# Kernel optimization log

Measured on AMD Instinct MI355X. Metric: run time of the kernel, lower is better.

## Reference

```python
import jax, jax.numpy as jnp
import numpy as np

E = 16          # ensemble_size
S = 64          # state_size
A = 32          # action_size
R = 1           # reward_size
I = S + A       # combined input size
HS = 64         # SubModel_state hidden
HR = 32         # SubModel_reward hidden
B = 16384       # batch


def setup_inputs() -> dict:
    key = jax.random.key(0)
    ks = jax.random.split(key, 10)

    def init_lin(k, fan_in, shape):
        bound = 1.0 / np.sqrt(fan_in)
        return jax.random.uniform(k, shape, jnp.float32, -bound, bound)

    return {
        "state": jax.random.normal(ks[0], (B, S), jnp.float32),
        "action": jax.random.normal(ks[1], (B, A), jnp.float32),
        # stacked ensemble state-model weights (torch Linear stores [out,in]; we use [in,out])
        "W1": init_lin(ks[2], I, (E, I, HS)),
        "b1": init_lin(ks[3], I, (E, HS)),
        "W2": init_lin(ks[4], HS, (E, HS, S)),
        "b2": init_lin(ks[5], HS, (E, S)),
        # stacked ensemble reward-model weights
        "rW1": init_lin(ks[6], I, (E, I, HR)),
        "rb1": init_lin(ks[7], I, (E, HR)),
        "rW2": init_lin(ks[8], HR, (E, HR, R)),
        "rb2": init_lin(ks[9], HR, (E, R)),
    }


def reference(state, action, W1, b1, W2, b2, rW1, rb1, rW2, rb2):
    x = jnp.concatenate([state, action], axis=1)  # [B, I]
    # state models: Linear -> ReLU -> Linear, all ensemble members in one batched GEMM
    h = jax.nn.relu(jnp.einsum("bi,eih->ebh", x, W1) + b1[:, None, :])  # [E, B, HS]
    pred_states = jnp.einsum("ebh,ehs->ebs", h, W2) + b2[:, None, :]    # [E, B, S]
    # reward models: Linear -> ReLU -> Linear -> clamp(-100, 200)
    hr = jax.nn.relu(jnp.einsum("bi,eih->ebh", x, rW1) + rb1[:, None, :])  # [E, B, HR]
    pred_rewards = jnp.einsum("ebh,ehr->ebr", hr, rW2) + rb2[:, None, :]   # [E, B, R]
    pred_rewards = jnp.clip(pred_rewards, -100.0, 200.0)
    return (pred_states, pred_rewards)
```

## Files before the change

### kernel.cpp

```cpp
#include <hip/hip_runtime.h>
#include <hip/hip_bf16.h>
#include <cstdint>
#include <cstddef>

#define Bsz 16384
#define Esz 16
#define Ssz 64
#define Asz 32
#define Isz 96
#define HSz 64
#define HRz 32

#define NTM 256
#define CHUNK 512
#define NTILE 8

typedef __attribute__((ext_vector_type(8))) short bf16x8;
typedef __attribute__((ext_vector_type(4))) short short4v;
typedef __attribute__((ext_vector_type(4))) float f32x4;

static __device__ __forceinline__ short f2bf(float f) {
    __hip_bfloat16 b = __float2bfloat16(f);
    return *reinterpret_cast<short*>(&b);
}
static __device__ __forceinline__ float bf2f(short s) {
    union { uint32_t u; float f; } v; v.u = ((uint32_t)(uint16_t)s) << 16; return v.f;
}
static __device__ __forceinline__ bf16x8 pack8(float4 lo, float4 hi) {
    bf16x8 r;
    r[0] = f2bf(lo.x); r[1] = f2bf(lo.y); r[2] = f2bf(lo.z); r[3] = f2bf(lo.w);
    r[4] = f2bf(hi.x); r[5] = f2bf(hi.y); r[6] = f2bf(hi.z); r[7] = f2bf(hi.w);
    return r;
}

__global__ __launch_bounds__(NTM, 2)
void fused_all(const float* __restrict__ state, const float* __restrict__ action,
               const float* __restrict__ W1, const float* __restrict__ b1,
               const float* __restrict__ W2, const float* __restrict__ b2,
               const float* __restrict__ rW1, const float* __restrict__ rb1,
               const float* __restrict__ rW2, const float* __restrict__ rb2,
               float* __restrict__ outS, float* __restrict__ outR)
{
    __shared__ __align__(16) short HT[4][16][68];

    const int bid = blockIdx.x;
    const int xcd = bid & 7;
    const int rem = bid >> 3;
    const int e   = rem & (Esz - 1);
    const int c0  = (xcd + 8 * (rem >> 4)) * CHUNK;

    const int w = threadIdx.x >> 6, lane = threadIdx.x & 63;
    const int lr = lane & 15, lg = lane >> 4;

    bf16x8 w1r[4][3], rw1r[2][3], w2r[4][2];
    {
        const float* base = W1 + (size_t)e * Isz * HSz;
        #pragma unroll
        for (int nt = 0; nt < 4; ++nt)
            #pragma unroll
            for (int kk = 0; kk < 3; ++kk) {
                const float* p = base + (kk * 32 + lg * 8) * HSz + nt * 16 + lr;
                bf16x8 r;
                #pragma unroll
                for (int t = 0; t < 8; ++t) r[t] = f2bf(p[t * HSz]);
                w1r[nt][kk] = r;
            }
    }
    {
        const float* base = rW1 + (size_t)e * Isz * HRz;
        #pragma unroll
        for (int nt = 0; nt < 2; ++nt)
            #pragma unroll
            for (int kk = 0; kk < 3; ++kk) {
                const float* p = base + (kk * 32 + lg * 8) * HRz + nt * 16 + lr;
                bf16x8 r;
                #pragma unroll
                for (int t = 0; t < 8; ++t) r[t] = f2bf(p[t * HRz]);
                rw1r[nt][kk] = r;
            }
    }
    {
        const float* base = W2 + (size_t)e * HSz * Ssz;
        #pragma unroll
        for (int nt = 0; nt < 4; ++nt)
            #pragma unroll
            for (int kk = 0; kk < 2; ++kk) {
                const float* p = base + (kk * 32 + lg * 8) * Ssz + nt * 16 + lr;
                bf16x8 r;
                #pragma unroll
                for (int t = 0; t < 8; ++t) r[t] = f2bf(p[t * Ssz]);
                w2r[nt][kk] = r;
            }
    }

    short4v b1p[4], b2p[4], rb1p[2], rw2p[2];
    #pragma unroll
    for (int nt = 0; nt < 4; ++nt) {
        float4 v1 = *(const float4*)&b1[e * HSz + nt * 16 + lg * 4];
        float4 v2 = *(const float4*)&b2[e * Ssz + nt * 16 + lg * 4];
        b1p[nt] = (short4v){ f2bf(v1.x), f2bf(v1.y), f2bf(v1.z), f2bf(v1.w) };
        b2p[nt] = (short4v){ f2bf(v2.x), f2bf(v2.y), f2bf(v2.z), f2bf(v2.w) };
    }
    #pragma unroll
    for (int nt = 0; nt < 2; ++nt) {
        float4 v1 = *(const float4*)&rb1[e * HRz + nt * 16 + lg * 4];
        float4 v2 = *(const float4*)&rW2[e * HRz + nt * 16 + lg * 4];
        rb1p[nt] = (short4v){ f2bf(v1.x), f2bf(v1.y), f2bf(v1.z), f2bf(v1.w) };
        rw2p[nt] = (short4v){ f2bf(v2.x), f2bf(v2.y), f2bf(v2.z), f2bf(v2.w) };
    }
    const float rb2s = rb2[e];

    const int row0 = c0 + w * 16 + lr;
    const float* sbase = state  + (size_t)row0 * Ssz + lg * 8;
    const float* abase = action + (size_t)row0 * Asz + lg * 8;

    float4 xs0 = *(const float4*)(sbase);
    float4 xs1 = *(const float4*)(sbase + 4);
    float4 xs2 = *(const float4*)(sbase + 32);
    float4 xs3 = *(const float4*)(sbase + 36);
    float4 xa0 = *(const float4*)(abase);
    float4 xa1 = *(const float4*)(abase + 4);
    bf16x8 a0 = pack8(xs0, xs1);
    bf16x8 a1 = pack8(xs2, xs3);
    bf16x8 a2 = pack8(xa0, xa1);

    #pragma unroll 1
    for (int t = 0; t < NTILE; ++t) {
        const int tn = (t + 1) & (NTILE - 1);
        const float* sp = sbase + (size_t)tn * 64 * Ssz;
        const float* ap = abase + (size_t)tn * 64 * Asz;
        float4 ns0 = *(const float4*)(sp);
        float4 ns1 = *(const float4*)(sp + 4);
        float4 ns2 = *(const float4*)(sp + 32);
        float4 ns3 = *(const float4*)(sp + 36);
        float4 na0 = *(const float4*)(ap);
        float4 na1 = *(const float4*)(ap + 4);

        f32x4 accS[4];
        #pragma unroll
        for (int nt = 0; nt < 4; ++nt) {
            f32x4 acc = (f32x4){ bf2f(b1p[nt][0]), bf2f(b1p[nt][1]),
                                 bf2f(b1p[nt][2]), bf2f(b1p[nt][3]) };
            acc = __builtin_amdgcn_mfma_f32_16x16x32_bf16(w1r[nt][0], a0, acc, 0, 0, 0);
            acc = __builtin_amdgcn_mfma_f32_16x16x32_bf16(w1r[nt][1], a1, acc, 0, 0, 0);
            acc = __builtin_amdgcn_mfma_f32_16x16x32_bf16(w1r[nt][2], a2, acc, 0, 0, 0);
            accS[nt] = acc;
        }
        f32x4 accR[2];
        #pragma unroll
        for (int nt = 0; nt < 2; ++nt) {
            f32x4 acc = (f32x4){ bf2f(rb1p[nt][0]), bf2f(rb1p[nt][1]),
                                 bf2f(rb1p[nt][2]), bf2f(rb1p[nt][3]) };
            acc = __builtin_amdgcn_mfma_f32_16x16x32_bf16(rw1r[nt][0], a0, acc, 0, 0, 0);
            acc = __builtin_amdgcn_mfma_f32_16x16x32_bf16(rw1r[nt][1], a1, acc, 0, 0, 0);
            acc = __builtin_amdgcn_mfma_f32_16x16x32_bf16(rw1r[nt][2], a2, acc, 0, 0, 0);
            accR[nt] = acc;
        }

        #pragma unroll
        for (int nt = 0; nt < 4; ++nt) {
            short4v p = { f2bf(fmaxf(accS[nt][0], 0.f)),
                          f2bf(fmaxf(accS[nt][1], 0.f)),
                          f2bf(fmaxf(accS[nt][2], 0.f)),
                          f2bf(fmaxf(accS[nt][3], 0.f)) };
            *(short4v*)&HT[w][lr][nt * 16 + lg * 4] = p;
        }

        float rp = 0.f;
        #pragma unroll
        for (int nt = 0; nt < 2; ++nt) {
            rp += fmaxf(accR[nt][0], 0.f) * bf2f(rw2p[nt][0]);
            rp += fmaxf(accR[nt][1], 0.f) * bf2f(rw2p[nt][1]);
            rp += fmaxf(accR[nt][2], 0.f) * bf2f(rw2p[nt][2]);
            rp += fmaxf(accR[nt][3], 0.f) * bf2f(rw2p[nt][3]);
        }
        rp += __shfl_xor(rp, 16);
        rp += __shfl_xor(rp, 32);
        if (lane < 16)
            __builtin_nontemporal_store(fminf(fmaxf(rp + rb2s, -100.f), 200.f),
                                        &outR[(size_t)e * Bsz + row0 + t * 64]);

        bf16x8 h0 = *(const bf16x8*)&HT[w][lr][lg * 8];
        bf16x8 h1 = *(const bf16x8*)&HT[w][lr][32 + lg * 8];
        #pragma unroll
        for (int nt = 0; nt < 4; ++nt) {
            f32x4 acc = (f32x4){ bf2f(b2p[nt][0]), bf2f(b2p[nt][1]),
                                 bf2f(b2p[nt][2]), bf2f(b2p[nt][3]) };
            acc = __builtin_amdgcn_mfma_f32_16x16x32_bf16(w2r[nt][0], h0, acc, 0, 0, 0);
            acc = __builtin_amdgcn_mfma_f32_16x16x32_bf16(w2r[nt][1], h1, acc, 0, 0, 0);
            __builtin_nontemporal_store(acc,
                (f32x4*)&outS[((size_t)e * Bsz + row0 + t * 64) * Ssz + nt * 16 + lg * 4]);
        }

        a0 = pack8(ns0, ns1);
        a1 = pack8(ns2, ns3);
        a2 = pack8(na0, na1);
    }
}

extern "C" void kernel_launch(void* const* d_in, const int* in_sizes, int n_in,
                              void* d_out, int out_size, void* d_ws, size_t ws_size,
                              hipStream_t stream) {
    const float* state  = (const float*)d_in[0];
    const float* action = (const float*)d_in[1];
    const float* W1  = (const float*)d_in[2];
    const float* b1  = (const float*)d_in[3];
    const float* W2  = (const float*)d_in[4];
    const float* b2  = (const float*)d_in[5];
    const float* rW1 = (const float*)d_in[6];
    const float* rb1 = (const float*)d_in[7];
    const float* rW2 = (const float*)d_in[8];
    const float* rb2 = (const float*)d_in[9];

    float* outS = (float*)d_out;
    float* outR = outS + (size_t)Esz * Bsz * Ssz;

    fused_all<<<Esz * (Bsz / CHUNK), NTM, 0, stream>>>(
        state, action, W1, b1, W2, b2, rW1, rb1, rW2, rb2, outS, outR);
}
```

Baseline: 27.27 us.

## Pre-pack ensemble weights into bf16 MFMA fragment layout in a prep kernel

Adds a small prep kernel that converts W1, rW1 and W2 to bf16 and lays them out in workspace in the exact per-lane fragment order the MFMA loop uses. The main kernel then loads each fragment with one 16-byte vector load instead of eight strided scalar fp32 loads plus conversions in every block. The aim is to cut redundant per-block weight-gathering latency, at the cost of an extra kernel launch and a workspace round trip. The reward output store also drops its nontemporal hint.

```diff
diff --git a/kernel.cpp b/kernel.cpp
--- a/kernel.cpp
+++ b/kernel.cpp
@@ -11,9 +11,11 @@
 #define HSz 64
 #define HRz 32
 
+#define PT 512
 #define NTM 256
 #define CHUNK 512
 #define NTILE 8
+#define WELEMS 13312
 
 typedef __attribute__((ext_vector_type(8))) short bf16x8;
 typedef __attribute__((ext_vector_type(4))) short short4v;
@@ -33,12 +35,35 @@
     return r;
 }
 
+__global__ void prep_w(const float* __restrict__ W1, const float* __restrict__ rW1,
+                       const float* __restrict__ W2, short* __restrict__ Wf) {
+    int idx = blockIdx.x * blockDim.x + threadIdx.x;
+    int e = idx / WELEMS, r = idx - e * WELEMS;
+    float v;
+    if (r < 6144) {
+        int nt = r / 1536, r2 = r % 1536, kk = r2 / 512, r3 = r2 % 512, l = r3 >> 3, t = r3 & 7;
+        int i = kk * 32 + (l >> 4) * 8 + t, h = nt * 16 + (l & 15);
+        v = W1[(size_t)e * Isz * HSz + i * HSz + h];
+    } else if (r < 9216) {
+        int r1 = r - 6144;
+        int nt = r1 / 1536, r2 = r1 % 1536, kk = r2 / 512, r3 = r2 % 512, l = r3 >> 3, t = r3 & 7;
+        int i = kk * 32 + (l >> 4) * 8 + t, h = nt * 16 + (l & 15);
+        v = rW1[(size_t)e * Isz * HRz + i * HRz + h];
+    } else {
+        int r1 = r - 9216;
+        int nt = r1 / 1024, r2 = r1 % 1024, kk = r2 / 512, r3 = r2 % 512, l = r3 >> 3, t = r3 & 7;
+        int hk = kk * 32 + (l >> 4) * 8 + t, s = nt * 16 + (l & 15);
+        v = W2[(size_t)e * HSz * Ssz + hk * Ssz + s];
+    }
+    Wf[idx] = f2bf(v);
+}
+
 __global__ __launch_bounds__(NTM, 2)
 void fused_all(const float* __restrict__ state, const float* __restrict__ action,
-               const float* __restrict__ W1, const float* __restrict__ b1,
-               const float* __restrict__ W2, const float* __restrict__ b2,
-               const float* __restrict__ rW1, const float* __restrict__ rb1,
-               const float* __restrict__ rW2, const float* __restrict__ rb2,
+               const short* __restrict__ Wf,
+               const float* __restrict__ b1, const float* __restrict__ b2,
+               const float* __restrict__ rb1, const float* __restrict__ rW2,
+               const float* __restrict__ rb2,
                float* __restrict__ outS, float* __restrict__ outR)
 {
     __shared__ __align__(16) short HT[4][16][68];
@@ -54,43 +79,22 @@
 
     bf16x8 w1r[4][3], rw1r[2][3], w2r[4][2];
     {
-        const float* base = W1 + (size_t)e * Isz * HSz;
+        const short* p = Wf + (size_t)e * WELEMS + lane * 8;
         #pragma unroll
         for (int nt = 0; nt < 4; ++nt)
             #pragma unroll
-            for (int kk = 0; kk < 3; ++kk) {
-                const float* p = base + (kk * 32 + lg * 8) * HSz + nt * 16 + lr;
-                bf16x8 r;
-                #pragma unroll
-                for (int t = 0; t < 8; ++t) r[t] = f2bf(p[t * HSz]);
-                w1r[nt][kk] = r;
-            }
-    }
-    {
-        const float* base = rW1 + (size_t)e * Isz * HRz;
+            for (int kk = 0; kk < 3; ++kk)
+                w1r[nt][kk] = *(const bf16x8*)(p + (nt * 3 + kk) * 512);
         #pragma unroll
         for (int nt = 0; nt < 2; ++nt)
             #pragma unroll
-            for (int kk = 0; kk < 3; ++kk) {
-                const float* p = base + (kk * 32 + lg * 8) * HRz + nt * 16 + lr;
-                bf16x8 r;
-                #pragma unroll
-                for (int t = 0; t < 8; ++t) r[t] = f2bf(p[t * HRz]);
-                rw1r[nt][kk] = r;
-            }
-    }
-    {
-        const float* base = W2 + (size_t)e * HSz * Ssz;
+            for (int kk = 0; kk < 3; ++kk)
+                rw1r[nt][kk] = *(const bf16x8*)(p + 6144 + (nt * 3 + kk) * 512);
         #pragma unroll
         for (int nt = 0; nt < 4; ++nt)
             #pragma unroll
-            for (int kk = 0; kk < 2; ++kk) {
-                const float* p = base + (kk * 32 + lg * 8) * Ssz + nt * 16 + lr;
-                bf16x8 r;
-                #pragma unroll
-                for (int t = 0; t < 8; ++t) r[t] = f2bf(p[t * Ssz]);
-                w2r[nt][kk] = r;
-            }
+            for (int kk = 0; kk < 2; ++kk)
+                w2r[nt][kk] = *(const bf16x8*)(p + 9216 + (nt * 2 + kk) * 512);
     }
 
     short4v b1p[4], b2p[4], rb1p[2], rw2p[2];
@@ -177,8 +181,7 @@
         rp += __shfl_xor(rp, 16);
         rp += __shfl_xor(rp, 32);
         if (lane < 16)
-            __builtin_nontemporal_store(fminf(fmaxf(rp + rb2s, -100.f), 200.f),
-                                        &outR[(size_t)e * Bsz + row0 + t * 64]);
+            outR[(size_t)e * Bsz + row0 + t * 64] = fminf(fmaxf(rp + rb2s, -100.f), 200.f);
 
         bf16x8 h0 = *(const bf16x8*)&HT[w][lr][lg * 8];
         bf16x8 h1 = *(const bf16x8*)&HT[w][lr][32 + lg * 8];
@@ -215,6 +218,9 @@
     float* outS = (float*)d_out;
     float* outR = outS + (size_t)Esz * Bsz * Ssz;
 
+    short* Wf = (short*)d_ws;
+
+    prep_w<<<(Esz * WELEMS) / PT, PT, 0, stream>>>(W1, rW1, W2, Wf);
     fused_all<<<Esz * (Bsz / CHUNK), NTM, 0, stream>>>(
-        state, action, W1, b1, W2, b2, rW1, rb1, rW2, rb2, outS, outR);
-}
+        state, action, Wf, b1, b2, rb1, rW2, rb2, outS, outR);
+}
```

After: 32.04 us. +17.5%, slower.

## Pre-convert inputs to bf16 and split reward model into separate blocks

Applied to the files above, without the earlier changes.

Adds a prep kernel that concatenates state and action and converts them to a bf16 workspace once, so the main kernel no longer re-reads fp32 inputs and repacks them for every ensemble member. The main kernel now runs the state-model and reward-model paths in separate blocks (512 state blocks plus 128 reward blocks), which lowers register pressure and raises the launch bound to 3 blocks per CU. The cost is an extra kernel launch and a workspace round trip, plus a possible imbalance between the two block types.

```diff
diff --git a/kernel.cpp b/kernel.cpp
--- a/kernel.cpp
+++ b/kernel.cpp
@@ -11,9 +11,14 @@
 #define HSz 64
 #define HRz 32
 
+#define PT 512
 #define NTM 256
 #define CHUNK 512
 #define NTILE 8
+#define NSB 512
+#define RCHUNK 2048
+#define RNTILE 32
+#define NRB 128
 
 typedef __attribute__((ext_vector_type(8))) short bf16x8;
 typedef __attribute__((ext_vector_type(4))) short short4v;
@@ -26,175 +31,197 @@
 static __device__ __forceinline__ float bf2f(short s) {
     union { uint32_t u; float f; } v; v.u = ((uint32_t)(uint16_t)s) << 16; return v.f;
 }
-static __device__ __forceinline__ bf16x8 pack8(float4 lo, float4 hi) {
+
+__global__ void prep_x(const float* __restrict__ state, const float* __restrict__ action,
+                       short* __restrict__ Xbf) {
+    int idx = blockIdx.x * blockDim.x + threadIdx.x;
+    int g = idx * 8;
+    int row = g / Isz, rem = g - row * Isz;
+    float4 lo, hi;
+    if (rem < Ssz) {
+        const float* p = state + (size_t)row * Ssz + rem;
+        lo = *(const float4*)(p); hi = *(const float4*)(p + 4);
+    } else {
+        const float* p = action + (size_t)row * Asz + (rem - Ssz);
+        lo = *(const float4*)(p); hi = *(const float4*)(p + 4);
+    }
     bf16x8 r;
     r[0] = f2bf(lo.x); r[1] = f2bf(lo.y); r[2] = f2bf(lo.z); r[3] = f2bf(lo.w);
     r[4] = f2bf(hi.x); r[5] = f2bf(hi.y); r[6] = f2bf(hi.z); r[7] = f2bf(hi.w);
-    return r;
-}
-
-__global__ __launch_bounds__(NTM, 2)
-void fused_all(const float* __restrict__ state, const float* __restrict__ action,
-               const float* __restrict__ W1, const float* __restrict__ b1,
-               const float* __restrict__ W2, const float* __restrict__ b2,
-               const float* __restrict__ rW1, const float* __restrict__ rb1,
-               const float* __restrict__ rW2, const float* __restrict__ rb2,
-               float* __restrict__ outS, float* __restrict__ outR)
+    *(bf16x8*)&Xbf[(size_t)row * Isz + rem] = r;
+}
+
+__global__ __launch_bounds__(NTM, 3)
+void fused_main(const short* __restrict__ Xbf,
+                const float* __restrict__ W1, const float* __restrict__ b1,
+                const float* __restrict__ W2, const float* __restrict__ b2,
+                const float* __restrict__ rW1, const float* __restrict__ rb1,
+                const float* __restrict__ rW2, const float* __restrict__ rb2,
+                float* __restrict__ outS, float* __restrict__ outR)
 {
     __shared__ __align__(16) short HT[4][16][68];
 
     const int bid = blockIdx.x;
-    const int xcd = bid & 7;
-    const int rem = bid >> 3;
-    const int e   = rem & (Esz - 1);
-    const int c0  = (xcd + 8 * (rem >> 4)) * CHUNK;
-
     const int w = threadIdx.x >> 6, lane = threadIdx.x & 63;
     const int lr = lane & 15, lg = lane >> 4;
 
-    bf16x8 w1r[4][3], rw1r[2][3], w2r[4][2];
-    {
-        const float* base = W1 + (size_t)e * Isz * HSz;
-        #pragma unroll
-        for (int nt = 0; nt < 4; ++nt)
-            #pragma unroll
-            for (int kk = 0; kk < 3; ++kk) {
-                const float* p = base + (kk * 32 + lg * 8) * HSz + nt * 16 + lr;
-                bf16x8 r;
+    if (bid < NSB) {
+        const int xcd = bid & 7;
+        const int rem = bid >> 3;
+        const int e   = rem & (Esz - 1);
+        const int c0  = (xcd + 8 * (rem >> 4)) * CHUNK;
+
+        bf16x8 w1r[4][3], w2r[4][2];
+        {
+            const float* base = W1 + (size_t)e * Isz * HSz;
+            #pragma unroll
+            for (int nt = 0; nt < 4; ++nt)
                 #pragma unroll
-                for (int t = 0; t < 8; ++t) r[t] = f2bf(p[t * HSz]);
-                w1r[nt][kk] = r;
-            }
-    }
-    {
-        const float* base = rW1 + (size_t)e * Isz * HRz;
-        #pragma unroll
-        for (int nt = 0; nt < 2; ++nt)
-            #pragma unroll
-            for (int kk = 0; kk < 3; ++kk) {
-                const float* p = base + (kk * 32 + lg * 8) * HRz + nt * 16 + lr;
-                bf16x8 r;
+                for (int kk = 0; kk < 3; ++kk) {
+                    const float* p = base + (kk * 32 + lg * 8) * HSz + nt * 16 + lr;
+                    bf16x8 r;
+                    #pragma unroll
+                    for (int t = 0; t < 8; ++t) r[t] = f2bf(p[t * HSz]);
+                    w1r[nt][kk] = r;
+                }
+        }
+        {
+            const float* base = W2 + (size_t)e * HSz * Ssz;
+            #pragma unroll
+            for (int nt = 0; nt < 4; ++nt)
                 #pragma unroll
-                for (int t = 0; t < 8; ++t) r[t] = f2bf(p[t * HRz]);
-                rw1r[nt][kk] = r;
-            }
-    }
-    {
-        const float* base = W2 + (size_t)e * HSz * Ssz;
-        #pragma unroll
-        for (int nt = 0; nt < 4; ++nt)
-            #pragma unroll
-            for (int kk = 0; kk < 2; ++kk) {
-                const float* p = base + (kk * 32 + lg * 8) * Ssz + nt * 16 + lr;
-                bf16x8 r;
-                #pragma unroll
-                for (int t = 0; t < 8; ++t) r[t] = f2bf(p[t * Ssz]);
-                w2r[nt][kk] = r;
-            }
-    }
-
-    short4v b1p[4], b2p[4], rb1p[2], rw2p[2];
-    #pragma unroll
-    for (int nt = 0; nt < 4; ++nt) {
-        float4 v1 = *(const float4*)&b1[e * HSz + nt * 16 + lg * 4];
-        float4 v2 = *(const float4*)&b2[e * Ssz + nt * 16 + lg * 4];
-        b1p[nt] = (short4v){ f2bf(v1.x), f2bf(v1.y), f2bf(v1.z), f2bf(v1.w) };
-        b2p[nt] = (short4v){ f2bf(v2.x), f2bf(v2.y), f2bf(v2.z), f2bf(v2.w) };
-    }
-    #pragma unroll
-    for (int nt = 0; nt < 2; ++nt) {
-        float4 v1 = *(const float4*)&rb1[e * HRz + nt * 16 + lg * 4];
-        float4 v2 = *(const float4*)&rW2[e * HRz + nt * 16 + lg * 4];
-        rb1p[nt] = (short4v){ f2bf(v1.x), f2bf(v1.y), f2bf(v1.z), f2bf(v1.w) };
-        rw2p[nt] = (short4v){ f2bf(v2.x), f2bf(v2.y), f2bf(v2.z), f2bf(v2.w) };
-    }
-    const float rb2s = rb2[e];
-
-    const int row0 = c0 + w * 16 + lr;
-    const float* sbase = state  + (size_t)row0 * Ssz + lg * 8;
-    const float* abase = action + (size_t)row0 * Asz + lg * 8;
-
-    float4 xs0 = *(const float4*)(sbase);
-    float4 xs1 = *(const float4*)(sbase + 4);
-    float4 xs2 = *(const float4*)(sbase + 32);
-    float4 xs3 = *(const float4*)(sbase + 36);
-    float4 xa0 = *(const float4*)(abase);
-    float4 xa1 = *(const float4*)(abase + 4);
-    bf16x8 a0 = pack8(xs0, xs1);
-    bf16x8 a1 = pack8(xs2, xs3);
-    bf16x8 a2 = pack8(xa0, xa1);
-
-    #pragma unroll 1
-    for (int t = 0; t < NTILE; ++t) {
-        const int tn = (t + 1) & (NTILE - 1);
-        const float* sp = sbase + (size_t)tn * 64 * Ssz;
-        const float* ap = abase + (size_t)tn * 64 * Asz;
-        float4 ns0 = *(const float4*)(sp);
-        float4 ns1 = *(const float4*)(sp + 4);
-        float4 ns2 = *(const float4*)(sp + 32);
-        float4 ns3 = *(const float4*)(sp + 36);
-        float4 na0 = *(const float4*)(ap);
-        float4 na1 = *(const float4*)(ap + 4);
-
-        f32x4 accS[4];
+                for (int kk = 0; kk < 2; ++kk) {
+                    const float* p = base + (kk * 32 + lg * 8) * Ssz + nt * 16 + lr;
+                    bf16x8 r;
+                    #pragma unroll
+                    for (int t = 0; t < 8; ++t) r[t] = f2bf(p[t * Ssz]);
+                    w2r[nt][kk] = r;
+                }
+        }
+        short4v b1p[4], b2p[4];
         #pragma unroll
         for (int nt = 0; nt < 4; ++nt) {
-            f32x4 acc = (f32x4){ bf2f(b1p[nt][0]), bf2f(b1p[nt][1]),
-                                 bf2f(b1p[nt][2]), bf2f(b1p[nt][3]) };
-            acc = __builtin_amdgcn_mfma_f32_16x16x32_bf16(w1r[nt][0], a0, acc, 0, 0, 0);
-            acc = __builtin_amdgcn_mfma_f32_16x16x32_bf16(w1r[nt][1], a1, acc, 0, 0, 0);
-            acc = __builtin_amdgcn_mfma_f32_16x16x32_bf16(w1r[nt][2], a2, acc, 0, 0, 0);
-            accS[nt] = acc;
-        }
-        f32x4 accR[2];
+            float4 v1 = *(const float4*)&b1[e * HSz + nt * 16 + lg * 4];
+            float4 v2 = *(const float4*)&b2[e * Ssz + nt * 16 + lg * 4];
+            b1p[nt] = (short4v){ f2bf(v1.x), f2bf(v1.y), f2bf(v1.z), f2bf(v1.w) };
+            b2p[nt] = (short4v){ f2bf(v2.x), f2bf(v2.y), f2bf(v2.z), f2bf(v2.w) };
+        }
+
+        const int row0 = c0 + w * 16 + lr;
+        const short* xbase = Xbf + (size_t)row0 * Isz + lg * 8;
+
+        bf16x8 a0 = *(const bf16x8*)(xbase);
+        bf16x8 a1 = *(const bf16x8*)(xbase + 32);
+        bf16x8 a2 = *(const bf16x8*)(xbase + 64);
+
+        #pragma unroll 1
+        for (int t = 0; t < NTILE; ++t) {
+            const int tn = (t + 1) & (NTILE - 1);
+            const short* xn = xbase + (size_t)tn * 64 * Isz;
+            bf16x8 n0 = *(const bf16x8*)(xn);
+            bf16x8 n1 = *(const bf16x8*)(xn + 32);
+            bf16x8 n2 = *(const bf16x8*)(xn + 64);
+
+            f32x4 accS[4];
+            #pragma unroll
+            for (int nt = 0; nt < 4; ++nt) {
+                f32x4 acc = (f32x4){ bf2f(b1p[nt][0]), bf2f(b1p[nt][1]),
+                                     bf2f(b1p[nt][2]), bf2f(b1p[nt][3]) };
+                acc = __builtin_amdgcn_mfma_f32_16x16x32_bf16(w1r[nt][0], a0, acc, 0, 0, 0);
+                acc = __builtin_amdgcn_mfma_f32_16x16x32_bf16(w1r[nt][1], a1, acc, 0, 0, 0);
+                acc = __builtin_amdgcn_mfma_f32_16x16x32_bf16(w1r[nt][2], a2, acc, 0, 0, 0);
+                accS[nt] = acc;
+            }
+            #pragma unroll
+            for (int nt = 0; nt < 4; ++nt) {
+                short4v p = { f2bf(fmaxf(accS[nt][0], 0.f)),
+                              f2bf(fmaxf(accS[nt][1], 0.f)),
+                              f2bf(fmaxf(accS[nt][2], 0.f)),
+                              f2bf(fmaxf(accS[nt][3], 0.f)) };
+                *(short4v*)&HT[w][lr][nt * 16 + lg * 4] = p;
+            }
+            bf16x8 h0 = *(const bf16x8*)&HT[w][lr][lg * 8];
+            bf16x8 h1 = *(const bf16x8*)&HT[w][lr][32 + lg * 8];
+            #pragma unroll
+            for (int nt = 0; nt < 4; ++nt) {
+                f32x4 acc = (f32x4){ bf2f(b2p[nt][0]), bf2f(b2p[nt][1]),
+                                     bf2f(b2p[nt][2]), bf2f(b2p[nt][3]) };
+                acc = __builtin_amdgcn_mfma_f32_16x16x32_bf16(w2r[nt][0], h0, acc, 0, 0, 0);
+                acc = __builtin_amdgcn_mfma_f32_16x16x32_bf16(w2r[nt][1], h1, acc, 0, 0, 0);
+                __builtin_nontemporal_store(acc,
+                    (f32x4*)&outS[((size_t)e * Bsz + row0 + t * 64) * Ssz + nt * 16 + lg * 4]);
+            }
+            a0 = n0; a1 = n1; a2 = n2;
+        }
+    } else {
+        const int rbid = bid - NSB;
+        const int e  = rbid & (Esz - 1);
+        const int c0 = (rbid >> 4) * RCHUNK;
+
+        bf16x8 rw1r[2][3];
+        {
+            const float* base = rW1 + (size_t)e * Isz * HRz;
+            #pragma unroll
+            for (int nt = 0; nt < 2; ++nt)
+                #pragma unroll
+                for (int kk = 0; kk < 3; ++kk) {
+                    const float* p = base + (kk * 32 + lg * 8) * HRz + nt * 16 + lr;
+                    bf16x8 r;
+                    #pragma unroll
+                    for (int t = 0; t < 8; ++t) r[t] = f2bf(p[t * HRz]);
+                    rw1r[nt][kk] = r;
+                }
+        }
+        short4v rb1p[2], rw2p[2];
         #pragma unroll
         for (int nt = 0; nt < 2; ++nt) {
-            f32x4 acc = (f32x4){ bf2f(rb1p[nt][0]), bf2f(rb1p[nt][1]),
-                                 bf2f(rb1p[nt][2]), bf2f(rb1p[nt][3]) };
-            acc = __builtin_amdgcn_mfma_f32_16x16x32_bf16(rw1r[nt][0], a0, acc, 0, 0, 0);
-            acc = __builtin_amdgcn_mfma_f32_16x16x32_bf16(rw1r[nt][1], a1, acc, 0, 0, 0);
-            acc = __builtin_amdgcn_mfma_f32_16x16x32_bf16(rw1r[nt][2], a2, acc, 0, 0, 0);
-            accR[nt] = acc;
-        }
-
-        #pragma unroll
-        for (int nt = 0; nt < 4; ++nt) {
-            short4v p = { f2bf(fmaxf(accS[nt][0], 0.f)),
-                          f2bf(fmaxf(accS[nt][1], 0.f)),
-                          f2bf(fmaxf(accS[nt][2], 0.f)),
-                          f2bf(fmaxf(accS[nt][3], 0.f)) };
-            *(short4v*)&HT[w][lr][nt * 16 + lg * 4] = p;
-        }
-
-        float rp = 0.f;
-        #pragma unroll
-        for (int nt = 0; nt < 2; ++nt) {
-            rp += fmaxf(accR[nt][0], 0.f) * bf2f(rw2p[nt][0]);
-            rp += fmaxf(accR[nt][1], 0.f) * bf2f(rw2p[nt][1]);
-            rp += fmaxf(accR[nt][2], 0.f) * bf2f(rw2p[nt][2]);
-            rp += fmaxf(accR[nt][3], 0.f) * bf2f(rw2p[nt][3]);
-        }
-        rp += __shfl_xor(rp, 16);
-        rp += __shfl_xor(rp, 32);
-        if (lane < 16)
-            __builtin_nontemporal_store(fminf(fmaxf(rp + rb2s, -100.f), 200.f),
-                                        &outR[(size_t)e * Bsz + row0 + t * 64]);
-
-        bf16x8 h0 = *(const bf16x8*)&HT[w][lr][lg * 8];
-        bf16x8 h1 = *(const bf16x8*)&HT[w][lr][32 + lg * 8];
-        #pragma unroll
-        for (int nt = 0; nt < 4; ++nt) {
-            f32x4 acc = (f32x4){ bf2f(b2p[nt][0]), bf2f(b2p[nt][1]),
-                                 bf2f(b2p[nt][2]), bf2f(b2p[nt][3]) };
-            acc = __builtin_amdgcn_mfma_f32_16x16x32_bf16(w2r[nt][0], h0, acc, 0, 0, 0);
-            acc = __builtin_amdgcn_mfma_f32_16x16x32_bf16(w2r[nt][1], h1, acc, 0, 0, 0);
-            __builtin_nontemporal_store(acc,
-                (f32x4*)&outS[((size_t)e * Bsz + row0 + t * 64) * Ssz + nt * 16 + lg * 4]);
-        }
-
-        a0 = pack8(ns0, ns1);
-        a1 = pack8(ns2, ns3);
-        a2 = pack8(na0, na1);
+            float4 v1 = *(const float4*)&rb1[e * HRz + nt * 16 + lg * 4];
+            float4 v2 = *(const float4*)&rW2[e * HRz + nt * 16 + lg * 4];
+            rb1p[nt] = (short4v){ f2bf(v1.x), f2bf(v1.y), f2bf(v1.z), f2bf(v1.w) };
+            rw2p[nt] = (short4v){ f2bf(v2.x), f2bf(v2.y), f2bf(v2.z), f2bf(v2.w) };
+        }
+        const float rb2s = rb2[e];
+
+        const int row0 = c0 + w * 16 + lr;
+        const short* xbase = Xbf + (size_t)row0 * Isz + lg * 8;
+
+        bf16x8 a0 = *(const bf16x8*)(xbase);
+        bf16x8 a1 = *(const bf16x8*)(xbase + 32);
+        bf16x8 a2 = *(const bf16x8*)(xbase + 64);
+
+        #pragma unroll 1
+        for (int t = 0; t < RNTILE; ++t) {
+            const int tn = (t + 1) & (RNTILE - 1);
+            const short* xn = xbase + (size_t)tn * 64 * Isz;
+            bf16x8 n0 = *(const bf16x8*)(xn);
+            bf16x8 n1 = *(const bf16x8*)(xn + 32);
+            bf16x8 n2 = *(const bf16x8*)(xn + 64);
+
+            f32x4 accR[2];
+            #pragma unroll
+            for (int nt = 0; nt < 2; ++nt) {
+                f32x4 acc = (f32x4){ bf2f(rb1p[nt][0]), bf2f(rb1p[nt][1]),
+                                     bf2f(rb1p[nt][2]), bf2f(rb1p[nt][3]) };
+                acc = __builtin_amdgcn_mfma_f32_16x16x32_bf16(rw1r[nt][0], a0, acc, 0, 0, 0);
+                acc = __builtin_amdgcn_mfma_f32_16x16x32_bf16(rw1r[nt][1], a1, acc, 0, 0, 0);
+                acc = __builtin_amdgcn_mfma_f32_16x16x32_bf16(rw1r[nt][2], a2, acc, 0, 0, 0);
+                accR[nt] = acc;
+            }
+            float rp = 0.f;
+            #pragma unroll
+            for (int nt = 0; nt < 2; ++nt) {
+                rp += fmaxf(accR[nt][0], 0.f) * bf2f(rw2p[nt][0]);
+                rp += fmaxf(accR[nt][1], 0.f) * bf2f(rw2p[nt][1]);
+                rp += fmaxf(accR[nt][2], 0.f) * bf2f(rw2p[nt][2]);
+                rp += fmaxf(accR[nt][3], 0.f) * bf2f(rw2p[nt][3]);
+            }
+            rp += __shfl_xor(rp, 16);
+            rp += __shfl_xor(rp, 32);
+            if (lane < 16)
+                __builtin_nontemporal_store(fminf(fmaxf(rp + rb2s, -100.f), 200.f),
+                                            &outR[(size_t)e * Bsz + row0 + t * 64]);
+            a0 = n0; a1 = n1; a2 = n2;
+        }
     }
 }
 
@@ -215,6 +242,9 @@
     float* outS = (float*)d_out;
     float* outR = outS + (size_t)Esz * Bsz * Ssz;
 
-    fused_all<<<Esz * (Bsz / CHUNK), NTM, 0, stream>>>(
-        state, action, W1, b1, W2, b2, rW1, rb1, rW2, rb2, outS, outR);
-}
+    short* Xbf = (short*)d_ws;
+
+    prep_x<<<(Bsz * Isz / 8) / PT, PT, 0, stream>>>(state, action, Xbf);
+    fused_main<<<NSB + NRB, NTM, 0, stream>>>(
+        Xbf, W1, b1, W2, b2, rW1, rb1, rW2, rb2, outS, outR);
+}
```

Measured after the change: 46.38 us. +70.0%, slower.
